# Optimization experiments

Measured on AMD Instinct MI355X. Metric: run time of the kernel, lower is better.

## Reference

```python
import jax, jax.numpy as jnp
import numpy as np

N_NODES = 50000
NEG_SLOPE = 0.2


def setup_inputs() -> dict:
    key = jax.random.key(0)
    k1, k2, k3, k4 = jax.random.split(key, 4)
    N, E, F, H, C = 50000, 800000, 128, 4, 32
    x = jax.random.normal(k1, (N, F), dtype=jnp.float32)
    edge_index = jax.random.randint(k2, (2, E), 0, N, dtype=jnp.int32)
    weight = jax.random.normal(k3, (F, H * C), dtype=jnp.float32) * 0.1  # glorot-ish scale
    att = jax.random.normal(k4, (1, H, 2 * C), dtype=jnp.float32) * 0.1
    bias = jnp.zeros((C,), dtype=jnp.float32)
    return {"x": x, "edge_index": edge_index, "weight": weight, "att": att, "bias": bias}


def reference(x, edge_index, weight, att, bias):
    N = x.shape[0]
    H, C2 = att.shape[1], att.shape[2]
    C = C2 // 2
    # linear projection -> [N, H, C]
    xw = jnp.matmul(x, weight).reshape(N, H, C)
    row, col = edge_index[0], edge_index[1]
    # per-edge attention logits: gather both endpoints, concat along channel
    x_i = xw[row]                     # [E, H, C]
    x_j = xw[col]                     # [E, H, C]
    cat_x = jnp.concatenate([x_i, x_j], axis=-1)      # [E, H, 2C]
    alpha = jnp.sum(cat_x * att, axis=-1)             # [E, H]
    alpha = jnp.where(alpha >= 0, alpha, NEG_SLOPE * alpha)  # leaky_relu
    # segment softmax grouped by row (source index, as in the torch code)
    seg_max = jax.ops.segment_max(alpha, row, num_segments=N)
    seg_max = jnp.where(jnp.isfinite(seg_max), seg_max, 0.0)
    alpha = jnp.exp(alpha - seg_max[row])
    seg_sum = jax.ops.segment_sum(alpha, row, num_segments=N)
    alpha = alpha / (seg_sum[row] + 1e-16)            # [E, H]
    # PyG propagate: message = alpha * x_j where x_j = x[edge_index[0]],
    # aggregated (scatter-add) into target = edge_index[1]
    msg = alpha[..., None] * xw[row]                  # [E, H, C]
    out = jax.ops.segment_sum(msg, col, num_segments=N)  # [N, H, C]
    out = out.mean(axis=1) + bias                     # concat=False -> head mean, + bias
    return out
```

## Files before the change

kernel.cpp:

```cpp
#include <hip/hip_runtime.h>
#include <hip/hip_fp16.h>

#define FDIM 128
#define HEADS 4
#define CD 32
#define BM 64
#define NBKT 256
#define SSUB 4
#define MAXNL 200

typedef __attribute__((ext_vector_type(8))) short bfrag;
typedef __attribute__((ext_vector_type(4))) float ffrag;

static __device__ __forceinline__ unsigned short f2bf(float v) {
    unsigned u = __float_as_uint(v);
    u += 0x7FFF + ((u >> 16) & 1);
    return (unsigned short)(u >> 16);
}
static __device__ __forceinline__ float bf2f(unsigned short u) {
    return __uint_as_float(((unsigned)u) << 16);
}

__global__ __launch_bounds__(256) void k_wsplit(const float* __restrict__ w,
                                                unsigned short* __restrict__ wt_hi,
                                                unsigned short* __restrict__ wt_lo)
{
    int i = blockIdx.x * 256 + threadIdx.x;
    float v = w[i];
    unsigned short h = f2bf(v);
    float r = v - bf2f(h);
    int k = i >> 7, n = i & 127;
    wt_hi[n * FDIM + k] = h;
    wt_lo[n * FDIM + k] = f2bf(r);
}

__global__ __launch_bounds__(256) void k_hist(const int* __restrict__ ei, int E, int N,
                                              int* __restrict__ cntT, int nch)
{
    __shared__ int h[NBKT];
    int t = threadIdx.x, chunk = blockIdx.x;
    h[t] = 0;
    __syncthreads();
    int e = chunk * 256 + t;
    if (e < E) atomicAdd(&h[(ei[e] * NBKT) / N], 1);
    __syncthreads();
    cntT[t * nch + chunk] = h[t];
}

__global__ __launch_bounds__(256) void k_scanA(const int* __restrict__ cntT,
                                               int* __restrict__ boffT,
                                               int* __restrict__ btot, int nch)
{
    __shared__ int ws[4];
    int t = threadIdx.x, lane = t & 63, w = t >> 6, b = blockIdx.x;
    int carry = 0;
    for (int c0 = 0; c0 < nch; c0 += 256) {
        int idx = c0 + t;
        int v = (idx < nch) ? cntT[b * nch + idx] : 0;
        int x = v;
#pragma unroll
        for (int d = 1; d < 64; d <<= 1) { int y = __shfl_up(x, d, 64); if (lane >= d) x += y; }
        if (lane == 63) ws[w] = x;
        __syncthreads();
        int woff = 0;
        for (int i = 0; i < w; i++) woff += ws[i];
        int tot = ws[0] + ws[1] + ws[2] + ws[3];
        if (idx < nch) boffT[b * nch + idx] = carry + woff + (x - v);
        carry += tot;
        __syncthreads();
    }
    if (t == 0) btot[b] = carry;
}

__global__ __launch_bounds__(256) void k_scanB(const int* __restrict__ btot,
                                               int* __restrict__ bbase, int E)
{
    __shared__ int ws[4];
    int t = threadIdx.x, lane = t & 63, w = t >> 6;
    int v = btot[t];
    int x = v;
#pragma unroll
    for (int d = 1; d < 64; d <<= 1) { int y = __shfl_up(x, d, 64); if (lane >= d) x += y; }
    if (lane == 63) ws[w] = x;
    __syncthreads();
    int woff = 0;
    for (int i = 0; i < w; i++) woff += ws[i];
    bbase[t] = woff + (x - v);
    if (t == 255) bbase[256] = E;
}

__global__ __launch_bounds__(256) void k_place(const int* __restrict__ ei, int E, int N,
                                               const int* __restrict__ boffT,
                                               const int* __restrict__ bbase,
                                               uint2* __restrict__ recs, int nch)
{
    __shared__ int sOff[NBKT];
    __shared__ int lcnt[NBKT];
    int t = threadIdx.x, chunk = blockIdx.x;
    sOff[t] = bbase[t] + boffT[t * nch + chunk];
    lcnt[t] = 0;
    __syncthreads();
    int e = chunk * 256 + t;
    if (e < E) {
        int r = ei[e], cl = ei[E + e];
        int b = (r * NBKT) / N;
        int pos = sOff[b] + atomicAdd(&lcnt[b], 1);
        recs[pos] = make_uint2((unsigned)r, (unsigned)cl);
    }
}

__global__ __launch_bounds__(256) void k_gemm(const float* __restrict__ x,
                                              const unsigned short* __restrict__ wt_hi,
                                              const unsigned short* __restrict__ wt_lo,
                                              const float* __restrict__ att,
                                              unsigned short* __restrict__ xwh,
                                              float* __restrict__ a_src,
                                              float* __restrict__ a_dst,
                                              float4* __restrict__ zero_base,
                                              int nz4, int N)
{
    __shared__ float accs[BM * 132];
    __shared__ float attl[HEADS * 2 * CD];
    int t = threadIdx.x;
    int row0 = blockIdx.x * BM;
    for (int i = blockIdx.x * 256 + t; i < nz4; i += gridDim.x * 256)
        zero_base[i] = make_float4(0.f, 0.f, 0.f, 0.f);
    attl[t] = att[t];

    int l = t & 63, wv = t >> 6;
    int la = l & 15, lr = l >> 4;
    int arow = row0 + wv * 16 + la;
    bool aval = arow < N;
    const float* xbase = x + (size_t)arow * FDIM + lr * 8;

    ffrag acc[8] = {};
#pragma unroll
    for (int ks = 0; ks < 4; ks++) {
        float xv[8] = {0.f, 0.f, 0.f, 0.f, 0.f, 0.f, 0.f, 0.f};
        if (aval) {
            float4 f0 = *(const float4*)(xbase + ks * 32);
            float4 f1 = *(const float4*)(xbase + ks * 32 + 4);
            xv[0] = f0.x; xv[1] = f0.y; xv[2] = f0.z; xv[3] = f0.w;
            xv[4] = f1.x; xv[5] = f1.y; xv[6] = f1.z; xv[7] = f1.w;
        }
        bfrag ah, al;
#pragma unroll
        for (int j = 0; j < 8; j++) {
            unsigned short h = f2bf(xv[j]);
            ah[j] = (short)h;
            al[j] = (short)f2bf(xv[j] - bf2f(h));
        }
        int boffk = ks * 32 + lr * 8;
#pragma unroll
        for (int ct = 0; ct < 8; ct++) {
            int o = (ct * 16 + la) * FDIM + boffk;
            bfrag bh = *(const bfrag*)(wt_hi + o);
            bfrag bl = *(const bfrag*)(wt_lo + o);
            acc[ct] = __builtin_amdgcn_mfma_f32_16x16x32_bf16(ah, bh, acc[ct], 0, 0, 0);
            acc[ct] = __builtin_amdgcn_mfma_f32_16x16x32_bf16(ah, bl, acc[ct], 0, 0, 0);
            acc[ct] = __builtin_amdgcn_mfma_f32_16x16x32_bf16(al, bh, acc[ct], 0, 0, 0);
        }
    }

#pragma unroll
    for (int i = 0; i < 4; i++) {
        int r = row0 + wv * 16 + lr * 4 + i;
        if (r < N) {
            uint2 pa, pb;
            pa.x = (unsigned)f2bf(acc[0][i]) | ((unsigned)f2bf(acc[2][i]) << 16);
            pa.y = (unsigned)f2bf(acc[4][i]) | ((unsigned)f2bf(acc[6][i]) << 16);
            pb.x = (unsigned)f2bf(acc[1][i]) | ((unsigned)f2bf(acc[3][i]) << 16);
            pb.y = (unsigned)f2bf(acc[5][i]) | ((unsigned)f2bf(acc[7][i]) << 16);
            *(uint2*)&xwh[(size_t)r * FDIM + la * 4] = pa;
            *(uint2*)&xwh[(size_t)r * FDIM + 64 + la * 4] = pb;
        }
    }
#pragma unroll
    for (int ct = 0; ct < 8; ct++)
#pragma unroll
        for (int i = 0; i < 4; i++)
            accs[(wv * 16 + lr * 4 + i) * 132 + ct * 16 + la] = acc[ct][i];
    __syncthreads();
    int row = t >> 2, h = t & 3;
    const float* ap = &attl[h * 2 * CD];
    const float* xr = &accs[row * 132 + h * CD];
    float s = 0.f, d = 0.f;
#pragma unroll 8
    for (int c = 0; c < CD; c++) { float v = xr[c]; s += v * ap[c]; d += v * ap[CD + c]; }
    int n = row0 + row;
    if (n < N) { a_src[n * 4 + h] = s; a_dst[n * 4 + h] = d; }
}

__global__ __launch_bounds__(256) void k_seg(const uint2* __restrict__ recs,
                                             const int* __restrict__ bbase,
                                             const float* __restrict__ a_src,
                                             const float* __restrict__ a_dst,
                                             float* __restrict__ seg_part, int N)
{
    __shared__ float segl[MAXNL * 4];
    int t = threadIdx.x;
    int b = blockIdx.x >> 2, s = blockIdx.x & 3;
    int ln0 = (b * N + NBKT - 1) / NBKT;
    int ln1 = ((b + 1) * N + NBKT - 1) / NBKT;
    int NL = ln1 - ln0;
    for (int i = t; i < NL * 4; i += 256) segl[i] = 0.f;
    __syncthreads();
    int lo = bbase[b], hi = bbase[b + 1];
    int slot = t >> 2, h = t & 3;
    for (int i = lo + s * 64 + slot; i < hi; i += 4 * 64) {
        uint2 rec = recs[i];
        int r = (int)rec.x, cl = (int)rec.y;
        float a = a_src[r * 4 + h] + a_dst[cl * 4 + h];
        a = a >= 0.f ? a : 0.2f * a;
        atomicAdd(&segl[(r - ln0) * 4 + h], __expf(a));
    }
    __syncthreads();
    float* op = seg_part + ((size_t)s * N + ln0) * 4;
    for (int i = t; i < NL * 4; i += 256) op[i] = segl[i];
}

__global__ void k_segsum(const float* __restrict__ sp, float* __restrict__ sinv, int N)
{
    int i = blockIdx.x * 256 + threadIdx.x;
    if (i >= N * 4) return;
    size_t st = (size_t)N * 4;
    float s = sp[i] + sp[st + i] + sp[2 * st + i] + sp[3 * st + i];
    sinv[i] = 0.25f / (s + 1e-16f);
}

__global__ __launch_bounds__(256) void k_scatter(const uint2* __restrict__ recs,
                                                 const float* __restrict__ a_src,
                                                 const float* __restrict__ a_dst,
                                                 const float* __restrict__ sinv,
                                                 const unsigned short* __restrict__ xwh,
                                                 __half2* __restrict__ out_acc2, int E)
{
    int t = threadIdx.x;
    int le = t >> 4, c2 = t & 15, lane = t & 63;
    int idx = blockIdx.x * 16 + le;
    if (idx >= E) return;
    uint2 rec = recs[idx];
    int r = (int)rec.x, cl = (int)rec.y;
    float av = 0.f;
    if (c2 < 4) {
        float a = a_src[r * 4 + c2] + a_dst[cl * 4 + c2];
        a = a >= 0.f ? a : 0.2f * a;
        av = __expf(a) * sinv[r * 4 + c2];
    }
    uint4 q = ((const uint4*)(xwh + (size_t)r * FDIM))[c2];
    float a0 = __shfl(av, (lane & 48) + 0, 64);
    float a1 = __shfl(av, (lane & 48) + 1, 64);
    float a2 = __shfl(av, (lane & 48) + 2, 64);
    float a3 = __shfl(av, (lane & 48) + 3, 64);
    float v0 = a0 * bf2f((unsigned short)(q.x & 0xFFFF)) + a1 * bf2f((unsigned short)(q.x >> 16))
             + a2 * bf2f((unsigned short)(q.y & 0xFFFF)) + a3 * bf2f((unsigned short)(q.y >> 16));
    float v1 = a0 * bf2f((unsigned short)(q.z & 0xFFFF)) + a1 * bf2f((unsigned short)(q.z >> 16))
             + a2 * bf2f((unsigned short)(q.w & 0xFFFF)) + a3 * bf2f((unsigned short)(q.w >> 16));
    unsafeAtomicAdd(&out_acc2[(size_t)cl * 16 + c2], __floats2half2_rn(v0, v1));
}

__global__ void k_final(const __half2* __restrict__ out_acc2, const float4* __restrict__ bias,
                        float4* __restrict__ out, int N)
{
    int i = blockIdx.x * 256 + threadIdx.x;
    if (i >= N * 8) return;
    float4 b = bias[i & 7];
    float2 f0 = __half22float2(out_acc2[i * 2]);
    float2 f1 = __half22float2(out_acc2[i * 2 + 1]);
    out[i] = make_float4(f0.x + b.x, f0.y + b.y, f1.x + b.z, f1.y + b.w);
}

extern "C" void kernel_launch(void* const* d_in, const int* in_sizes, int n_in,
                              void* d_out, int out_size, void* d_ws, size_t ws_size,
                              hipStream_t stream)
{
    const float* x    = (const float*)d_in[0];
    const int*   ei   = (const int*)d_in[1];
    const float* w    = (const float*)d_in[2];
    const float* att  = (const float*)d_in[3];
    const float* bias = (const float*)d_in[4];
    float* out = (float*)d_out;
    int N = in_sizes[0] / FDIM;
    int E = in_sizes[1] / 2;
    int nch = (E + 255) / 256;

    unsigned short* xwh = (unsigned short*)d_ws;
    uint2* recs  = (uint2*)(xwh + (size_t)N * FDIM);
    float* a_src = (float*)(recs + (size_t)E);
    float* a_dst = a_src + (size_t)N * HEADS;
    float* sinv  = a_dst + (size_t)N * HEADS;
    float* seg_part = sinv + (size_t)N * HEADS;
    __half2* out_acc2 = (__half2*)(seg_part + (size_t)SSUB * N * HEADS);
    unsigned short* wt_hi = (unsigned short*)(out_acc2 + (size_t)N * 16);
    unsigned short* wt_lo = wt_hi + FDIM * FDIM;
    int* btot  = (int*)(wt_lo + FDIM * FDIM);
    int* bbase = btot + NBKT;
    int* cntT  = bbase + NBKT + 8;
    int* boffT = cntT + (size_t)NBKT * nch;

    int nz4 = N * 4;

    k_wsplit<<<(FDIM * FDIM) / 256, 256, 0, stream>>>(w, wt_hi, wt_lo);
    k_hist<<<nch, 256, 0, stream>>>(ei, E, N, cntT, nch);
    k_scanA<<<NBKT, 256, 0, stream>>>(cntT, boffT, btot, nch);
    k_scanB<<<1, 256, 0, stream>>>(btot, bbase, E);
    k_place<<<nch, 256, 0, stream>>>(ei, E, N, boffT, bbase, recs, nch);
    k_gemm<<<(N + BM - 1) / BM, 256, 0, stream>>>(x, wt_hi, wt_lo, att, xwh, a_src, a_dst,
                                                  (float4*)out_acc2, nz4, N);
    k_seg<<<NBKT * SSUB, 256, 0, stream>>>(recs, bbase, a_src, a_dst, seg_part, N);
    k_segsum<<<(N * HEADS + 255) / 256, 256, 0, stream>>>(seg_part, sinv, N);
    k_scatter<<<(E + 15) / 16, 256, 0, stream>>>(recs, a_src, a_dst, sinv, xwh, out_acc2, E);
    k_final<<<(N * 8 + 255) / 256, 256, 0, stream>>>(out_acc2, (const float4*)bias,
                                                     (float4*)out, N);
}
```

Before: 220.3 us.

## Bucket edges by destination and compute softmax sums with global atomics

Edges are now bucketed by destination (col) instead of source. The per-bucket shared-memory segment-sum kernel and its reduction kernel are replaced by a flat per-edge kernel that atomically adds exp logits into a global per-source sum, zeroed together with the output accumulator. The scatter kernel becomes a grid-stride loop over 8 destination groups so concurrent atomics land in a narrower address range, and it computes the normalisation inline. This removes two launches and the partial-sum buffer, but adds contended global float atomics on source rows and relies on a fixed per-group grid size estimate.

```diff
diff --git a/kernel.cpp b/kernel.cpp
--- a/kernel.cpp
+++ b/kernel.cpp
@@ -6,8 +6,6 @@
 #define CD 32
 #define BM 64
 #define NBKT 256
-#define SSUB 4
-#define MAXNL 200
 
 typedef __attribute__((ext_vector_type(8))) short bfrag;
 typedef __attribute__((ext_vector_type(4))) float ffrag;
@@ -42,7 +40,7 @@
     h[t] = 0;
     __syncthreads();
     int e = chunk * 256 + t;
-    if (e < E) atomicAdd(&h[(ei[e] * NBKT) / N], 1);
+    if (e < E) atomicAdd(&h[(ei[E + e] * NBKT) / N], 1);
     __syncthreads();
     cntT[t * nch + chunk] = h[t];
 }
@@ -103,7 +101,7 @@
     int e = chunk * 256 + t;
     if (e < E) {
         int r = ei[e], cl = ei[E + e];
-        int b = (r * NBKT) / N;
+        int b = (cl * NBKT) / N;
         int pos = sOff[b] + atomicAdd(&lcnt[b], 1);
         recs[pos] = make_uint2((unsigned)r, (unsigned)cl);
     }
@@ -191,72 +189,54 @@
     if (n < N) { a_src[n * 4 + h] = s; a_dst[n * 4 + h] = d; }
 }
 
-__global__ __launch_bounds__(256) void k_seg(const uint2* __restrict__ recs,
-                                             const int* __restrict__ bbase,
-                                             const float* __restrict__ a_src,
-                                             const float* __restrict__ a_dst,
-                                             float* __restrict__ seg_part, int N)
-{
-    __shared__ float segl[MAXNL * 4];
-    int t = threadIdx.x;
-    int b = blockIdx.x >> 2, s = blockIdx.x & 3;
-    int ln0 = (b * N + NBKT - 1) / NBKT;
-    int ln1 = ((b + 1) * N + NBKT - 1) / NBKT;
-    int NL = ln1 - ln0;
-    for (int i = t; i < NL * 4; i += 256) segl[i] = 0.f;
-    __syncthreads();
-    int lo = bbase[b], hi = bbase[b + 1];
-    int slot = t >> 2, h = t & 3;
-    for (int i = lo + s * 64 + slot; i < hi; i += 4 * 64) {
-        uint2 rec = recs[i];
-        int r = (int)rec.x, cl = (int)rec.y;
-        float a = a_src[r * 4 + h] + a_dst[cl * 4 + h];
-        a = a >= 0.f ? a : 0.2f * a;
-        atomicAdd(&segl[(r - ln0) * 4 + h], __expf(a));
-    }
-    __syncthreads();
-    float* op = seg_part + ((size_t)s * N + ln0) * 4;
-    for (int i = t; i < NL * 4; i += 256) op[i] = segl[i];
-}
-
-__global__ void k_segsum(const float* __restrict__ sp, float* __restrict__ sinv, int N)
-{
-    int i = blockIdx.x * 256 + threadIdx.x;
-    if (i >= N * 4) return;
-    size_t st = (size_t)N * 4;
-    float s = sp[i] + sp[st + i] + sp[2 * st + i] + sp[3 * st + i];
-    sinv[i] = 0.25f / (s + 1e-16f);
+__global__ __launch_bounds__(256) void k_esum(const int* __restrict__ ei, int E,
+                                              const float* __restrict__ a_src,
+                                              const float* __restrict__ a_dst,
+                                              float* __restrict__ seg)
+{
+    int gid = blockIdx.x * 256 + threadIdx.x;
+    if (gid >= E * HEADS) return;
+    int e = gid >> 2, h = gid & 3;
+    int r = ei[e], cl = ei[E + e];
+    float a = a_src[r * 4 + h] + a_dst[cl * 4 + h];
+    a = a >= 0.f ? a : 0.2f * a;
+    atomicAdd(&seg[r * 4 + h], __expf(a));
 }
 
 __global__ __launch_bounds__(256) void k_scatter(const uint2* __restrict__ recs,
+                                                 const int* __restrict__ bbase,
                                                  const float* __restrict__ a_src,
                                                  const float* __restrict__ a_dst,
-                                                 const float* __restrict__ sinv,
+                                                 const float* __restrict__ seg,
                                                  const unsigned short* __restrict__ xwh,
-                                                 __half2* __restrict__ out_acc2, int E)
+                                                 __half2* __restrict__ out_acc2, int bpg)
 {
     int t = threadIdx.x;
     int le = t >> 4, c2 = t & 15, lane = t & 63;
-    int idx = blockIdx.x * 16 + le;
-    if (idx >= E) return;
-    uint2 rec = recs[idx];
-    int r = (int)rec.x, cl = (int)rec.y;
-    float av = 0.f;
-    if (c2 < 4) {
-        float a = a_src[r * 4 + c2] + a_dst[cl * 4 + c2];
-        a = a >= 0.f ? a : 0.2f * a;
-        av = __expf(a) * sinv[r * 4 + c2];
-    }
-    uint4 q = ((const uint4*)(xwh + (size_t)r * FDIM))[c2];
-    float a0 = __shfl(av, (lane & 48) + 0, 64);
-    float a1 = __shfl(av, (lane & 48) + 1, 64);
-    float a2 = __shfl(av, (lane & 48) + 2, 64);
-    float a3 = __shfl(av, (lane & 48) + 3, 64);
-    float v0 = a0 * bf2f((unsigned short)(q.x & 0xFFFF)) + a1 * bf2f((unsigned short)(q.x >> 16))
-             + a2 * bf2f((unsigned short)(q.y & 0xFFFF)) + a3 * bf2f((unsigned short)(q.y >> 16));
-    float v1 = a0 * bf2f((unsigned short)(q.z & 0xFFFF)) + a1 * bf2f((unsigned short)(q.z >> 16))
-             + a2 * bf2f((unsigned short)(q.w & 0xFFFF)) + a3 * bf2f((unsigned short)(q.w >> 16));
-    unsafeAtomicAdd(&out_acc2[(size_t)cl * 16 + c2], __floats2half2_rn(v0, v1));
+    int j = blockIdx.x & 7;
+    int lo = bbase[j * 32], hi = bbase[(j + 1) * 32];
+    for (int chunk = blockIdx.x >> 3; lo + chunk * 16 < hi; chunk += bpg) {
+        int idx = lo + chunk * 16 + le;
+        bool v = idx < hi;
+        uint2 rec = recs[v ? idx : lo];
+        int r = (int)rec.x, cl = (int)rec.y;
+        float av = 0.f;
+        if (v && c2 < 4) {
+            float a = a_src[r * 4 + c2] + a_dst[cl * 4 + c2];
+            a = a >= 0.f ? a : 0.2f * a;
+            av = __expf(a) * 0.25f / (seg[r * 4 + c2] + 1e-16f);
+        }
+        uint4 q = ((const uint4*)(xwh + (size_t)r * FDIM))[c2];
+        float a0 = __shfl(av, (lane & 48) + 0, 64);
+        float a1 = __shfl(av, (lane & 48) + 1, 64);
+        float a2 = __shfl(av, (lane & 48) + 2, 64);
+        float a3 = __shfl(av, (lane & 48) + 3, 64);
+        float v0 = a0 * bf2f((unsigned short)(q.x & 0xFFFF)) + a1 * bf2f((unsigned short)(q.x >> 16))
+                 + a2 * bf2f((unsigned short)(q.y & 0xFFFF)) + a3 * bf2f((unsigned short)(q.y >> 16));
+        float v1 = a0 * bf2f((unsigned short)(q.z & 0xFFFF)) + a1 * bf2f((unsigned short)(q.z >> 16))
+                 + a2 * bf2f((unsigned short)(q.w & 0xFFFF)) + a3 * bf2f((unsigned short)(q.w >> 16));
+        if (v) unsafeAtomicAdd(&out_acc2[(size_t)cl * 16 + c2], __floats2half2_rn(v0, v1));
+    }
 }
 
 __global__ void k_final(const __half2* __restrict__ out_acc2, const float4* __restrict__ bias,
@@ -288,9 +268,8 @@
     uint2* recs  = (uint2*)(xwh + (size_t)N * FDIM);
     float* a_src = (float*)(recs + (size_t)E);
     float* a_dst = a_src + (size_t)N * HEADS;
-    float* sinv  = a_dst + (size_t)N * HEADS;
-    float* seg_part = sinv + (size_t)N * HEADS;
-    __half2* out_acc2 = (__half2*)(seg_part + (size_t)SSUB * N * HEADS);
+    float* seg   = a_dst + (size_t)N * HEADS;
+    __half2* out_acc2 = (__half2*)(seg + (size_t)N * HEADS);
     unsigned short* wt_hi = (unsigned short*)(out_acc2 + (size_t)N * 16);
     unsigned short* wt_lo = wt_hi + FDIM * FDIM;
     int* btot  = (int*)(wt_lo + FDIM * FDIM);
@@ -298,7 +277,8 @@
     int* cntT  = bbase + NBKT + 8;
     int* boffT = cntT + (size_t)NBKT * nch;
 
-    int nz4 = N * 4;
+    int nz4 = N * 5;
+    int bpg = (E / 8 + E / 64 + 15) / 16;
 
     k_wsplit<<<(FDIM * FDIM) / 256, 256, 0, stream>>>(w, wt_hi, wt_lo);
     k_hist<<<nch, 256, 0, stream>>>(ei, E, N, cntT, nch);
@@ -306,10 +286,9 @@
     k_scanB<<<1, 256, 0, stream>>>(btot, bbase, E);
     k_place<<<nch, 256, 0, stream>>>(ei, E, N, boffT, bbase, recs, nch);
     k_gemm<<<(N + BM - 1) / BM, 256, 0, stream>>>(x, wt_hi, wt_lo, att, xwh, a_src, a_dst,
-                                                  (float4*)out_acc2, nz4, N);
-    k_seg<<<NBKT * SSUB, 256, 0, stream>>>(recs, bbase, a_src, a_dst, seg_part, N);
-    k_segsum<<<(N * HEADS + 255) / 256, 256, 0, stream>>>(seg_part, sinv, N);
-    k_scatter<<<(E + 15) / 16, 256, 0, stream>>>(recs, a_src, a_dst, sinv, xwh, out_acc2, E);
+                                                  (float4*)seg, nz4, N);
+    k_esum<<<(E * HEADS + 255) / 256, 256, 0, stream>>>(ei, E, a_src, a_dst, seg);
+    k_scatter<<<8 * bpg, 256, 0, stream>>>(recs, bbase, a_src, a_dst, seg, xwh, out_acc2, bpg);
     k_final<<<(N * 8 + 255) / 256, 256, 0, stream>>>(out_acc2, (const float4*)bias,
                                                      (float4*)out, N);
 }
```

After: 254.6 us. 1.16x slower.
